# Performance work log

Measured on AMD Instinct MI355X. Metric: run time of the kernel, lower is better.

The kernel has to match this reference:

```python
import jax, jax.numpy as jnp
import numpy as np

N_ENT = 100000
N_REL = 16
DIM = 128
N_LAYERS = 2
N_BASES = 4
N_EDGES = 640000
BATCH = 1024
N_NEG = 64
BN_EPS = 1e-5


def setup_inputs() -> dict:
    key = jax.random.key(0)
    ks = jax.random.split(key, 16)
    inp = {
        'head_idx': jax.random.randint(ks[0], (BATCH,), 0, N_ENT),
        'relation_idx': jax.random.randint(ks[1], (BATCH,), 0, N_REL),
        'tail_idx': jax.random.randint(ks[2], (BATCH,), 0, N_ENT),
        'negative_idx': jax.random.randint(ks[3], (BATCH, N_NEG), 0, N_ENT),
        'edge_index': jax.random.randint(ks[4], (2, N_EDGES), 0, N_ENT),
        'edge_type': jax.random.randint(ks[5], (N_EDGES,), 0, N_REL),
        # learned parameters (xavier-ish scaling)
        'entity_table': jax.random.normal(ks[6], (N_ENT, DIM), jnp.float32) * 0.02,
        'relation_table': jax.random.normal(ks[7], (N_REL, DIM), jnp.float32) * 0.02,
        'bases': jax.random.normal(ks[8], (N_LAYERS, N_BASES, DIM, DIM), jnp.float32) * (1.0 / np.sqrt(DIM)),
        'coeffs': jax.random.normal(ks[9], (N_LAYERS, N_REL, N_BASES), jnp.float32) * 0.5,
        'w_sl': jax.random.normal(ks[10], (N_LAYERS, DIM, DIM), jnp.float32) * (1.0 / np.sqrt(DIM)),
        'b_sl': jnp.zeros((N_LAYERS, DIM), jnp.float32),
        'gamma': jnp.ones((N_LAYERS, DIM), jnp.float32),
        'beta': jnp.zeros((N_LAYERS, DIM), jnp.float32),
    }
    return inp


def _encode(entity_table, bases, coeffs, w_sl, b_sl, gamma, beta, edge_index, edge_type):
    src, dst = edge_index[0], edge_index[1]
    n = entity_table.shape[0]
    # degree normalization (same dst for every layer)
    deg = jnp.zeros((n,), entity_table.dtype).at[dst].add(1.0)
    deg = jnp.maximum(deg, 1.0)[:, None]
    x = entity_table
    for l in range(N_LAYERS):
        # basis decomposition: W[r] = sum_b coeff[r,b] * bases[b]
        W = jnp.einsum('rb,bij->rij', coeffs[l], bases[l])  # [R, d, d]
        out = x @ w_sl[l] + b_sl[l]  # self-loop linear
        # transform all nodes under every relation once, then gather per edge
        H = jnp.einsum('nd,rdf->rnf', x, W)  # [R, N, d]
        msg = H[edge_type, src]  # [E, d]
        out = out.at[dst].add(msg)
        out = out / deg
        # BatchNorm1d (training mode: biased batch stats over nodes)
        mu = jnp.mean(out, axis=0)
        var = jnp.var(out, axis=0)
        out = (out - mu) * jax.lax.rsqrt(var + BN_EPS) * gamma[l] + beta[l]
        x = jax.nn.relu(out)
    return x


def reference(head_idx, relation_idx, tail_idx, negative_idx, edge_index, edge_type,
              entity_table, relation_table, bases, coeffs, w_sl, b_sl, gamma, beta):
    ent = _encode(entity_table, bases, coeffs, w_sl, b_sl, gamma, beta, edge_index, edge_type)
    head = ent[head_idx]                      # [B, d]
    rel = relation_table[relation_idx]        # [B, d]
    tail = ent[tail_idx]                      # [B, d]
    neg = ent[negative_idx]                   # [B, K, d]
    d_pos = head + rel - tail
    pos_score = -jnp.sqrt(jnp.sum(d_pos * d_pos, axis=-1))
    d_neg = (head + rel)[:, None, :] - neg
    neg_score = -jnp.sqrt(jnp.sum(d_neg * d_neg, axis=-1))
    return pos_score, neg_score
```

## Files before the change

kernel.cpp:

```cpp
#include <hip/hip_runtime.h>
#include <stdint.h>

#define N_ENTS  100000
#define N_RELS  16
#define DIM     128
#define NB      4
#define TILE_U  10240
#define NEDGE   640000
#define BATCH   1024
#define NNEG    64
#define BN_EPS  1e-5f
#define BCAP    64
#define NPB     32
#define NBLK2   3125
#define CONVX_BLKS 6250
#define CONVP_BLKS 652

#define P_REL    0
#define P_BASES  2048
#define P_COEFF  133120
#define P_WSL    133248
#define P_BSL    166016
#define P_GAMMA  166272
#define P_BETA   166528
#define P_TOTAL  166784

typedef unsigned int uint;
typedef short short8 __attribute__((ext_vector_type(8)));
typedef float f4 __attribute__((ext_vector_type(4)));

__device__ __forceinline__ float bf2f(unsigned short u) {
    return __uint_as_float(((unsigned int)u) << 16);
}
__device__ __forceinline__ float bflo(unsigned int u) { return __uint_as_float(u << 16); }
__device__ __forceinline__ float bfhi(unsigned int u) { return __uint_as_float(u & 0xffff0000u); }
__device__ __forceinline__ unsigned short f2bf(float f) {
    unsigned int x = __float_as_uint(f);
    x += 0x7fffu + ((x >> 16) & 1u);
    return (unsigned short)(x >> 16);
}
__device__ __forceinline__ unsigned int pack2(float a, float b) {
    return (unsigned int)f2bf(a) | ((unsigned int)f2bf(b) << 16);
}

__device__ __forceinline__ int bf16_like(unsigned int h) {
    unsigned int m = h & 0x7FFFu;
    return (m == 0u) || (m >= 0x2D00u && m < 0x4400u);
}
__global__ __launch_bounds__(256) void k_detect(const unsigned int* __restrict__ ent,
                                                int* __restrict__ flag) {
    __shared__ int cnt[256];
    unsigned int u = ent[threadIdx.x];
    cnt[threadIdx.x] = bf16_like(u & 0xFFFFu) & bf16_like(u >> 16);
    __syncthreads();
    for (int s = 128; s > 0; s >>= 1) {
        if (threadIdx.x < s) cnt[threadIdx.x] += cnt[threadIdx.x + s];
        __syncthreads();
    }
    if (threadIdx.x == 0) flag[0] = (cnt[0] >= 140) ? 1 : 0;
}

__device__ __forceinline__ unsigned short cvt1(const void* src, int i, int isbf) {
    return isbf ? ((const unsigned short*)src)[i] : f2bf(((const float*)src)[i]);
}
__global__ __launch_bounds__(256) void k_conv(
    const void* __restrict__ src, unsigned short* __restrict__ xrow,
    const void* __restrict__ rtab, const void* __restrict__ bases,
    const void* __restrict__ coeffs, const void* __restrict__ wsl,
    const void* __restrict__ bsl, const void* __restrict__ gamma,
    const void* __restrict__ beta,
    unsigned short* __restrict__ par, const int* __restrict__ flag)
{
    const int isbf = flag[0];
    if (blockIdx.x < CONVX_BLKS) {
        if (isbf) return;
        const int kc = threadIdx.x >> 4, r = threadIdx.x & 15;
        const int n = blockIdx.x * 16 + r;
        const size_t e0 = (size_t)n * DIM + kc * 8;
        const float4 f0 = *(const float4*)((const float*)src + e0);
        const float4 f1 = *(const float4*)((const float*)src + e0 + 4);
        uint4 w;
        w.x = pack2(f0.x, f0.y); w.y = pack2(f0.z, f0.w);
        w.z = pack2(f1.x, f1.y); w.w = pack2(f1.z, f1.w);
        *(uint4*)(xrow + e0) = w;
        return;
    }
    const int i = (blockIdx.x - CONVX_BLKS) * 256 + threadIdx.x;
    if (i >= P_TOTAL) return;
    unsigned short v;
    if      (i < P_BASES)  v = cvt1(rtab,   i - P_REL,    isbf);
    else if (i < P_COEFF)  v = cvt1(bases,  i - P_BASES,  isbf);
    else if (i < P_WSL)    v = cvt1(coeffs, i - P_COEFF,  isbf);
    else if (i < P_BSL)    v = cvt1(wsl,    i - P_WSL,    isbf);
    else if (i < P_GAMMA)  v = cvt1(bsl,    i - P_BSL,    isbf);
    else if (i < P_BETA)   v = cvt1(gamma,  i - P_GAMMA,  isbf);
    else                   v = cvt1(beta,   i - P_BETA,   isbf);
    par[i] = v;
}

__global__ __launch_bounds__(256) void k_fillB(const int* __restrict__ src, const int* __restrict__ dst,
                                               const int* __restrict__ et, int* __restrict__ cnt,
                                               uint* __restrict__ bucket) {
    const int e = blockIdx.x * 256 + threadIdx.x;
    const int d = dst[e];
    const int p = atomicAdd(&cnt[d], 1);
    if (p < BCAP) bucket[(size_t)d * BCAP + p] = (uint)src[e] | ((uint)et[e] << 20);
}

__global__ __launch_bounds__(256) void k_transw2(const unsigned short* __restrict__ par,
                                                 unsigned short* __restrict__ WtT,
                                                 float* __restrict__ cf32) {
    if (blockIdx.x == 80) {
        const int i = threadIdx.x;
        if (i < 2 * 17 * 4) {
            const int l = i / 68, rem = i - l * 68, r = rem >> 2, b = rem & 3;
            cf32[i] = (r < N_RELS) ? bf2f(par[P_COEFF + l * N_RELS * NB + r * NB + b]) : 0.f;
        }
        return;
    }
    const int i = blockIdx.x * 256 + threadIdx.x;
    const int l = i / 10240;
    const int rem = i - l * 10240;
    const int jt2 = rem / 1280;
    const int rem2 = rem - jt2 * 1280;
    const int kc = rem2 >> 4, r = rem2 & 15;
    const int n = jt2 * 16 + r;
    unsigned short v[8];
#pragma unroll
    for (int e = 0; e < 8; ++e) {
        const int k = kc * 8 + e;
        v[e] = (k < DIM)
            ? par[P_WSL + l * DIM * DIM + k * DIM + n]
            : par[P_BASES + l * NB * DIM * DIM + (k - DIM) * DIM + n];
    }
    *(uint4*)(WtT + (size_t)l * 81920 + (size_t)jt2 * TILE_U + (size_t)kc * 128 + r * 8) = *(uint4*)v;
}

__global__ __launch_bounds__(256, 4) void k_fused(
    const uint* __restrict__ bucket, const int* __restrict__ cnt,
    const float* __restrict__ cf, const unsigned short* __restrict__ xin,
    const void* __restrict__ ent, const int* __restrict__ flag, const int lay,
    const float* __restrict__ stp, const unsigned short* __restrict__ gprev,
    const unsigned short* __restrict__ bprev,
    const unsigned short* __restrict__ wtT, const unsigned short* __restrict__ bsl,
    unsigned short* __restrict__ out, float* __restrict__ pstats)
{
    __shared__ unsigned short Ash[NPB * 640];
    const int tid = threadIdx.x;
    const int wave = tid >> 6, lane = tid & 63;
    const int n0 = blockIdx.x * NPB;
    const float inv_n = 1.0f / (float)N_ENTS;

    const unsigned short* __restrict__ xs =
        (lay == 0 && flag[0]) ? (const unsigned short*)ent : xin;

    float gnA = 1.f, ofA = 0.f, gnB = 1.f, ofB = 0.f, flr = -3.0e38f;
    if (lay) {
        const int f0 = lane * 2, f1 = f0 + 1;
        const float mu0 = stp[f0] * inv_n, mu1 = stp[f1] * inv_n;
        const float va0 = stp[DIM + f0] * inv_n - mu0 * mu0;
        const float va1 = stp[DIM + f1] * inv_n - mu1 * mu1;
        gnA = bf2f(gprev[f0]) * rsqrtf(va0 + BN_EPS); ofA = bf2f(bprev[f0]) - mu0 * gnA;
        gnB = bf2f(gprev[f1]) * rsqrtf(va1 + BN_EPS); ofB = bf2f(bprev[f1]) - mu1 * gnB;
        flr = 0.f;
    }

    {
        const int r = tid >> 3, c = tid & 7;
        const size_t e0 = (size_t)(n0 + r) * DIM + c * 8;
        uint4 v0 = *(const uint4*)(xs + e0);
        uint4 v1 = *(const uint4*)(xs + e0 + 64);
        if (lay) {
            uint vv[8] = {v0.x, v0.y, v0.z, v0.w, v1.x, v1.y, v1.z, v1.w};
#pragma unroll
            for (int p = 0; p < 8; ++p) {
                const int f0 = c * 8 + (p >> 2) * 64 + (p & 3) * 2;
                const float mu0 = stp[f0] * inv_n, mu1 = stp[f0 + 1] * inv_n;
                const float va0 = stp[DIM + f0] * inv_n - mu0 * mu0;
                const float va1 = stp[DIM + f0 + 1] * inv_n - mu1 * mu1;
                const float g0 = bf2f(gprev[f0]) * rsqrtf(va0 + BN_EPS);
                const float g1 = bf2f(gprev[f0 + 1]) * rsqrtf(va1 + BN_EPS);
                const float o0 = bf2f(bprev[f0]) - mu0 * g0;
                const float o1 = bf2f(bprev[f0 + 1]) - mu1 * g1;
                const float w0 = fmaxf(fmaf(bflo(vv[p]), g0, o0), 0.f);
                const float w1 = fmaxf(fmaf(bfhi(vv[p]), g1, o1), 0.f);
                vv[p] = pack2(w0, w1);
            }
            v0.x = vv[0]; v0.y = vv[1]; v0.z = vv[2]; v0.w = vv[3];
            v1.x = vv[4]; v1.y = vv[5]; v1.z = vv[6]; v1.w = vv[7];
        }
        const int byte0 = (r * 1280 + c * 16) ^ ((r & 7) << 4);
        *(uint4*)((char*)Ash + byte0) = v0;
        *(uint4*)((char*)Ash + byte0 + 128) = v1;
    }

    const uint* __restrict__ x32 = (const uint*)xs;
    const int mybase = n0 + wave * 8;
    for (int pr = 0; pr < 4; ++pr) {
        const int na = mybase + pr * 2;
        int ca = cnt[na];     if (ca > BCAP) ca = BCAP;
        int cb = cnt[na + 1]; if (cb > BCAP) cb = BCAP;
        const int qm = ((ca > cb ? ca : cb) + 7) >> 3;
        float aLo[2][NB] = {{0.f,0.f,0.f,0.f},{0.f,0.f,0.f,0.f}};
        float aHi[2][NB] = {{0.f,0.f,0.f,0.f},{0.f,0.f,0.f,0.f}};
        const uint4* __restrict__ bk = (const uint4*)(bucket + (size_t)na * BCAP);
        for (int j = 0; j < qm; ++j) {
            uint rec[2][8];
            uint xw[2][8];
            const int b8 = j * 8;
#pragma unroll
            for (int h = 0; h < 2; ++h) {
                const int cn = h ? cb : ca;
                if (b8 < cn) {
                    const uint4 r0 = bk[h * 16 + j * 2];
                    const uint4 r1 = bk[h * 16 + j * 2 + 1];
                    rec[h][0] = r0.x; rec[h][1] = r0.y; rec[h][2] = r0.z; rec[h][3] = r0.w;
                    rec[h][4] = r1.x; rec[h][5] = r1.y; rec[h][6] = r1.z; rec[h][7] = r1.w;
#pragma unroll
                    for (int s = 0; s < 8; ++s) {
                        uint rr = (uint)__builtin_amdgcn_readfirstlane((int)rec[h][s]);
                        if (b8 + s >= cn) rr = 0x01000000u;
                        rec[h][s] = rr;
                        xw[h][s] = x32[(size_t)(rr & 0xFFFFFu) * 64 + lane];
                    }
                }
            }
#pragma unroll
            for (int h = 0; h < 2; ++h) {
                const int cn = h ? cb : ca;
                if (b8 < cn) {
#pragma unroll
                    for (int s = 0; s < 8; ++s) {
                        const int rel = (int)(rec[h][s] >> 20);
                        const float4 cc = *(const float4*)(cf + rel * 4);
                        const float xl = fmaxf(fmaf(bflo(xw[h][s]), gnA, ofA), flr);
                        const float xh = fmaxf(fmaf(bfhi(xw[h][s]), gnB, ofB), flr);
                        aLo[h][0] = fmaf(cc.x, xl, aLo[h][0]);
                        aHi[h][0] = fmaf(cc.x, xh, aHi[h][0]);
                        aLo[h][1] = fmaf(cc.y, xl, aLo[h][1]);
                        aHi[h][1] = fmaf(cc.y, xh, aHi[h][1]);
                        aLo[h][2] = fmaf(cc.z, xl, aLo[h][2]);
                        aHi[h][2] = fmaf(cc.z, xh, aHi[h][2]);
                        aLo[h][3] = fmaf(cc.w, xl, aLo[h][3]);
                        aHi[h][3] = fmaf(cc.w, xh, aHi[h][3]);
                    }
                }
            }
        }
#pragma unroll
        for (int h = 0; h < 2; ++h) {
            const int ra = wave * 8 + pr * 2 + h;
            const int swz = (ra & 7) << 4;
#pragma unroll
            for (int b = 0; b < NB; ++b) {
                const int byte = (ra * 1280 + 256 + b * 256 + lane * 4) ^ swz;
                *(uint*)((char*)Ash + byte) = pack2(aLo[h][b], aHi[h][b]);
            }
        }
    }

    const int quad = lane >> 4, l16 = lane & 15;
    f4 acc[2][2];
#pragma unroll
    for (int i = 0; i < 2; ++i)
#pragma unroll
        for (int j = 0; j < 2; ++j)
#pragma unroll
            for (int r = 0; r < 4; ++r) acc[i][j][r] = 0.f;

    const unsigned short* __restrict__ pB0 = wtT + (size_t)(2 * wave) * TILE_U + quad * 128 + l16 * 8;
    const unsigned short* __restrict__ pB1 = pB0 + TILE_U;
    const char* Ab = (const char*)Ash;
    const int swz = (l16 & 7) << 4;
    const int b0e = (l16 * 1280 + quad * 16) ^ swz;
    const int b0o = (l16 * 1280 + 64 + quad * 16) ^ swz;
    const int b1e = ((l16 + 16) * 1280 + quad * 16) ^ swz;
    const int b1o = ((l16 + 16) * 1280 + 64 + quad * 16) ^ swz;

    short8 xa0, xa1, xb0, xb1, ya0, ya1, yb0, yb1;
#define FLDA(P, s) \
    P##a0 = *(const short8*)(Ab + (((s) & 1) ? b0o : b0e) + ((s) >> 1) * 128); \
    P##a1 = *(const short8*)(Ab + (((s) & 1) ? b1o : b1e) + ((s) >> 1) * 128);
#define FLDB(P, s) \
    P##b0 = *(const short8*)(pB0 + (s) * 512); \
    P##b1 = *(const short8*)(pB1 + (s) * 512);
#define FLD(P, s) FLDA(P, s) FLDB(P, s)
#define FMM(P) \
    acc[0][0] = __builtin_amdgcn_mfma_f32_16x16x32_bf16(P##a0, P##b0, acc[0][0], 0, 0, 0); \
    acc[0][1] = __builtin_amdgcn_mfma_f32_16x16x32_bf16(P##a0, P##b1, acc[0][1], 0, 0, 0); \
    acc[1][0] = __builtin_amdgcn_mfma_f32_16x16x32_bf16(P##a1, P##b0, acc[1][0], 0, 0, 0); \
    acc[1][1] = __builtin_amdgcn_mfma_f32_16x16x32_bf16(P##a1, P##b1, acc[1][1], 0, 0, 0);

    FLDB(x, 0) FLDB(y, 1)
    __syncthreads();
    FLDA(x, 0) FLDA(y, 1)
    FMM(x) FLD(x, 2)
    FMM(y) FLD(y, 3)
    FMM(x) FLD(x, 4)
    FMM(y) FLD(y, 5)
    FMM(x) FLD(x, 6)
    FMM(y) FLD(y, 7)
    FMM(x) FLD(x, 8)
    FMM(y) FLD(y, 9)
    FMM(x) FLD(x, 10)
    FMM(y) FLD(y, 11)
    FMM(x) FLD(x, 12)
    FMM(y) FLD(y, 13)
    FMM(x) FLD(x, 14)
    FMM(y) FLD(y, 15)
    FMM(x) FLD(x, 16)
    FMM(y) FLD(y, 17)
    FMM(x) FLD(x, 18)
    FMM(y) FLD(y, 19)
    FMM(x)
    FMM(y)
#undef FLDA
#undef FLDB
#undef FLD
#undef FMM

    float ssum[2] = {0.f, 0.f}, sssq[2] = {0.f, 0.f};
#pragma unroll
    for (int m = 0; m < 2; ++m) {
#pragma unroll
        for (int r = 0; r < 4; ++r) {
            const int row = n0 + m * 16 + quad * 4 + r;
            const float rdeg = 1.0f / fmaxf((float)cnt[row], 1.0f);
#pragma unroll
            for (int n = 0; n < 2; ++n) {
                const int col = (2 * wave + n) * 16 + l16;
                const float o = (acc[m][n][r] + bf2f(bsl[col])) * rdeg;
                out[(size_t)row * DIM + col] = f2bf(o);
                ssum[n] += o;
                sssq[n] += o * o;
            }
        }
    }
#pragma unroll
    for (int n = 0; n < 2; ++n) {
        float s = ssum[n], q2 = sssq[n];
        s += __shfl_xor(s, 16, 64);  s += __shfl_xor(s, 32, 64);
        q2 += __shfl_xor(q2, 16, 64); q2 += __shfl_xor(q2, 32, 64);
        if (quad == 0) {
            const int col = (2 * wave + n) * 16 + l16;
            pstats[(size_t)blockIdx.x * 256 + col] = s;
            pstats[(size_t)blockIdx.x * 256 + 128 + col] = q2;
        }
    }
}

__global__ __launch_bounds__(256) void k_stats(const float* __restrict__ pstats,
                                               float* __restrict__ st) {
    const int o = threadIdx.x;
    const int b0 = blockIdx.x * 25;
    float s = 0.f;
    for (int b = b0; b < b0 + 25; ++b)
        s += pstats[(size_t)b * 256 + o];
    atomicAdd(&st[o], s);
}

__global__ __launch_bounds__(256) void k_score(
    const int* __restrict__ head, const int* __restrict__ rel,
    const int* __restrict__ tail, const int* __restrict__ negi,
    const unsigned short* __restrict__ emb, const unsigned short* __restrict__ rtab,
    const float* __restrict__ st1, const unsigned short* __restrict__ gm1,
    const unsigned short* __restrict__ bt1,
    void* __restrict__ outp, const int* __restrict__ flag)
{
    const int wave = threadIdx.x >> 6, lane = threadIdx.x & 63;
    const int w = blockIdx.x * 4 + wave;
    const float inv_n = 1.0f / (float)N_ENTS;
    const int f0 = lane * 2, f1 = f0 + 1;
    const float mu0 = st1[f0] * inv_n, mu1 = st1[f1] * inv_n;
    const float va0 = st1[DIM + f0] * inv_n - mu0 * mu0;
    const float va1 = st1[DIM + f1] * inv_n - mu1 * mu1;
    const float g0 = bf2f(gm1[f0]) * rsqrtf(va0 + BN_EPS);
    const float g1 = bf2f(gm1[f1]) * rsqrtf(va1 + BN_EPS);
    const float o0 = bf2f(bt1[f0]) - mu0 * g0;
    const float o1 = bf2f(bt1[f1]) - mu1 * g1;

    int i, t;
    if (w < BATCH) { i = w; t = tail[w]; }
    else { const int w2 = w - BATCH; i = w2 >> 6; t = negi[w2]; }
    const uint hv = ((const uint*)emb)[(size_t)head[i] * 64 + lane];
    const uint rv = ((const uint*)rtab)[(size_t)rel[i] * 64 + lane];
    const uint tv = ((const uint*)emb)[(size_t)t * 64 + lane];
    const float h0 = fmaxf(fmaf(bflo(hv), g0, o0), 0.f);
    const float h1 = fmaxf(fmaf(bfhi(hv), g1, o1), 0.f);
    const float t0 = fmaxf(fmaf(bflo(tv), g0, o0), 0.f);
    const float t1 = fmaxf(fmaf(bfhi(tv), g1, o1), 0.f);
    const float d0 = (h0 + bflo(rv)) - t0;
    const float d1 = (h1 + bfhi(rv)) - t1;
    float s = d0 * d0 + d1 * d1;
#pragma unroll
    for (int m = 32; m >= 1; m >>= 1) s += __shfl_xor(s, m, 64);
    if (lane == 0) {
        const float v = -sqrtf(s);
        if (flag[0]) ((unsigned short*)outp)[w] = f2bf(v);
        else         ((float*)outp)[w] = v;
    }
}

extern "C" void kernel_launch(void* const* d_in, const int* in_sizes, int n_in,
                              void* d_out, int out_size, void* d_ws, size_t ws_size,
                              hipStream_t stream)
{
    const int* head = (const int*)d_in[0];
    const int* rel  = (const int*)d_in[1];
    const int* tail = (const int*)d_in[2];
    const int* negi = (const int*)d_in[3];
    const int* eidx = (const int*)d_in[4];
    const int* etyp = (const int*)d_in[5];
    const void* ent_tab = d_in[6];
    const void* rtab_in = d_in[7];
    const void* bases_in = d_in[8];
    const void* coeffs_in = d_in[9];
    const void* wsl_in = d_in[10];
    const void* bsl_in = d_in[11];
    const void* gamma_in = d_in[12];
    const void* beta_in = d_in[13];

    char* ws = (char*)d_ws;
    size_t off = 0;
    auto alloc = [&](size_t bytes) -> char* {
        char* p = ws + off;
        off += (bytes + 511) & ~(size_t)511;
        return p;
    };
    int* flag            = (int*)alloc(4);
    int* cnt             = (int*)alloc((size_t)N_ENTS * 4);
    uint* bucket         = (uint*)alloc((size_t)N_ENTS * BCAP * 4);
    unsigned short* xrow = (unsigned short*)alloc((size_t)N_ENTS * DIM * 2);
    unsigned short* outA = (unsigned short*)alloc((size_t)N_ENTS * DIM * 2);
    unsigned short* outB = (unsigned short*)alloc((size_t)N_ENTS * DIM * 2);
    unsigned short* par  = (unsigned short*)alloc((size_t)P_TOTAL * 2);
    unsigned short* WtT  = (unsigned short*)alloc((size_t)2 * 81920 * 2);
    float* cf32          = (float*)alloc((size_t)2 * 17 * 4 * 4);
    float* pstats        = (float*)alloc((size_t)NBLK2 * 256 * 4);
    float* stats         = (float*)alloc(2 * 2 * DIM * 4);
    (void)ws_size; (void)in_sizes; (void)n_in; (void)out_size;

    const int* esrc = eidx;
    const int* edst = eidx + NEDGE;

    k_detect<<<1, 256, 0, stream>>>((const unsigned int*)ent_tab, flag);

    k_conv<<<CONVX_BLKS + CONVP_BLKS, 256, 0, stream>>>(
        ent_tab, xrow, rtab_in, bases_in, coeffs_in, wsl_in, bsl_in, gamma_in, beta_in,
        par, flag);
    k_transw2<<<81, 256, 0, stream>>>(par, WtT, cf32);

    hipMemsetAsync(cnt, 0, (size_t)N_ENTS * 4, stream);
    hipMemsetAsync(stats, 0, 2 * 2 * DIM * 4, stream);

    k_fillB<<<NEDGE / 256, 256, 0, stream>>>(esrc, edst, etyp, cnt, bucket);

    for (int l = 0; l < 2; ++l) {
        const unsigned short* bl = par + P_BSL + l * DIM;
        const unsigned short* wt = WtT + (size_t)l * 81920;
        const float* cf = cf32 + l * 68;

        k_fused<<<NBLK2, 256, 0, stream>>>(
            bucket, cnt, cf,
            l ? outA : xrow, ent_tab, flag, l,
            stats , par + P_GAMMA, par + P_BETA,
            wt, bl, l ? outB : outA, pstats);
        k_stats<<<125, 256, 0, stream>>>(pstats, stats + l * 2 * DIM);
    }

    k_score<<<(BATCH + BATCH * NNEG) / 4, 256, 0, stream>>>(
        head, rel, tail, negi, outB, par + P_REL,
        stats + 2 * DIM, par + P_GAMMA + DIM, par + P_BETA + DIM,
        d_out, flag);
}
```

Baseline: 354.0 us.

## Template fused layer kernel on layer and gather four nodes per iteration

Makes the layer index a template parameter, so the first layer skips the BN/ReLU transform in the gather loop and the floor trick goes away. Each wave now gathers neighbour rows for four nodes per iteration instead of two, which puts more independent global loads in flight to hide gather latency. The launch bounds also drop the min-blocks hint. The cost is higher register pressure from the 4x8 staging arrays and accumulators, which may reduce occupancy. Imbalanced degrees across the four nodes can also waste iterations.

After: 408.4 us. +15.4%, slower.

```diff
diff --git a/kernel.cpp b/kernel.cpp
--- a/kernel.cpp
+++ b/kernel.cpp
@@ -11,6 +11,7 @@
 #define NNEG    64
 #define BN_EPS  1e-5f
 #define BCAP    64
+#define SENTR   0x01000000u
 #define NPB     32
 #define NBLK2   3125
 #define CONVX_BLKS 6250
@@ -136,10 +137,11 @@
     *(uint4*)(WtT + (size_t)l * 81920 + (size_t)jt2 * TILE_U + (size_t)kc * 128 + r * 8) = *(uint4*)v;
 }
 
-__global__ __launch_bounds__(256, 4) void k_fused(
+template<int LAY>
+__global__ __launch_bounds__(256) void k_fused(
     const uint* __restrict__ bucket, const int* __restrict__ cnt,
     const float* __restrict__ cf, const unsigned short* __restrict__ xin,
-    const void* __restrict__ ent, const int* __restrict__ flag, const int lay,
+    const void* __restrict__ ent, const int* __restrict__ flag,
     const float* __restrict__ stp, const unsigned short* __restrict__ gprev,
     const unsigned short* __restrict__ bprev,
     const unsigned short* __restrict__ wtT, const unsigned short* __restrict__ bsl,
@@ -152,17 +154,16 @@
     const float inv_n = 1.0f / (float)N_ENTS;
 
     const unsigned short* __restrict__ xs =
-        (lay == 0 && flag[0]) ? (const unsigned short*)ent : xin;
-
-    float gnA = 1.f, ofA = 0.f, gnB = 1.f, ofB = 0.f, flr = -3.0e38f;
-    if (lay) {
+        (LAY == 0 && flag[0]) ? (const unsigned short*)ent : xin;
+
+    float gnA = 1.f, ofA = 0.f, gnB = 1.f, ofB = 0.f;
+    if (LAY) {
         const int f0 = lane * 2, f1 = f0 + 1;
         const float mu0 = stp[f0] * inv_n, mu1 = stp[f1] * inv_n;
         const float va0 = stp[DIM + f0] * inv_n - mu0 * mu0;
         const float va1 = stp[DIM + f1] * inv_n - mu1 * mu1;
         gnA = bf2f(gprev[f0]) * rsqrtf(va0 + BN_EPS); ofA = bf2f(bprev[f0]) - mu0 * gnA;
         gnB = bf2f(gprev[f1]) * rsqrtf(va1 + BN_EPS); ofB = bf2f(bprev[f1]) - mu1 * gnB;
-        flr = 0.f;
     }
 
     {
@@ -170,7 +171,7 @@
         const size_t e0 = (size_t)(n0 + r) * DIM + c * 8;
         uint4 v0 = *(const uint4*)(xs + e0);
         uint4 v1 = *(const uint4*)(xs + e0 + 64);
-        if (lay) {
+        if (LAY) {
             uint vv[8] = {v0.x, v0.y, v0.z, v0.w, v1.x, v1.y, v1.z, v1.w};
 #pragma unroll
             for (int p = 0; p < 8; ++p) {
@@ -196,65 +197,82 @@
 
     const uint* __restrict__ x32 = (const uint*)xs;
     const int mybase = n0 + wave * 8;
-    for (int pr = 0; pr < 4; ++pr) {
-        const int na = mybase + pr * 2;
-        int ca = cnt[na];     if (ca > BCAP) ca = BCAP;
-        int cb = cnt[na + 1]; if (cb > BCAP) cb = BCAP;
-        const int qm = ((ca > cb ? ca : cb) + 7) >> 3;
-        float aLo[2][NB] = {{0.f,0.f,0.f,0.f},{0.f,0.f,0.f,0.f}};
-        float aHi[2][NB] = {{0.f,0.f,0.f,0.f},{0.f,0.f,0.f,0.f}};
-        const uint4* __restrict__ bk = (const uint4*)(bucket + (size_t)na * BCAP);
+    for (int pp = 0; pp < 2; ++pp) {
+        const int naA = mybase + pp * 4;
+        const int naB = naA + 2;
+        int cA0 = cnt[naA];     if (cA0 > BCAP) cA0 = BCAP;
+        int cA1 = cnt[naA + 1]; if (cA1 > BCAP) cA1 = BCAP;
+        int cB0 = cnt[naB];     if (cB0 > BCAP) cB0 = BCAP;
+        int cB1 = cnt[naB + 1]; if (cB1 > BCAP) cB1 = BCAP;
+        const int qm0 = ((cA0 > cA1 ? cA0 : cA1) + 7) >> 3;
+        const int qm1 = ((cB0 > cB1 ? cB0 : cB1) + 7) >> 3;
+        const int qm = qm0 > qm1 ? qm0 : qm1;
+        float accLo[4][NB] = {{0.f,0.f,0.f,0.f},{0.f,0.f,0.f,0.f},
+                              {0.f,0.f,0.f,0.f},{0.f,0.f,0.f,0.f}};
+        float accHi[4][NB] = {{0.f,0.f,0.f,0.f},{0.f,0.f,0.f,0.f},
+                              {0.f,0.f,0.f,0.f},{0.f,0.f,0.f,0.f}};
+        const uint4* __restrict__ bkA = (const uint4*)(bucket + (size_t)naA * BCAP);
+        const uint4* __restrict__ bkB = (const uint4*)(bucket + (size_t)naB * BCAP);
         for (int j = 0; j < qm; ++j) {
-            uint rec[2][8];
-            uint xw[2][8];
             const int b8 = j * 8;
-#pragma unroll
-            for (int h = 0; h < 2; ++h) {
-                const int cn = h ? cb : ca;
+            uint rec[4][8];
+            uint xw[4][8];
+            const int cns[4] = {cA0, cA1, cB0, cB1};
+#pragma unroll
+            for (int g = 0; g < 4; ++g) {
+                const int cn = cns[g];
                 if (b8 < cn) {
+                    const uint4* bk = (g < 2) ? bkA : bkB;
+                    const int h = g & 1;
                     const uint4 r0 = bk[h * 16 + j * 2];
                     const uint4 r1 = bk[h * 16 + j * 2 + 1];
-                    rec[h][0] = r0.x; rec[h][1] = r0.y; rec[h][2] = r0.z; rec[h][3] = r0.w;
-                    rec[h][4] = r1.x; rec[h][5] = r1.y; rec[h][6] = r1.z; rec[h][7] = r1.w;
+                    rec[g][0] = r0.x; rec[g][1] = r0.y; rec[g][2] = r0.z; rec[g][3] = r0.w;
+                    rec[g][4] = r1.x; rec[g][5] = r1.y; rec[g][6] = r1.z; rec[g][7] = r1.w;
 #pragma unroll
                     for (int s = 0; s < 8; ++s) {
-                        uint rr = (uint)__builtin_amdgcn_readfirstlane((int)rec[h][s]);
-                        if (b8 + s >= cn) rr = 0x01000000u;
-                        rec[h][s] = rr;
-                        xw[h][s] = x32[(size_t)(rr & 0xFFFFFu) * 64 + lane];
+                        uint rr = (uint)__builtin_amdgcn_readfirstlane((int)rec[g][s]);
+                        if (b8 + s >= cn) rr = SENTR;
+                        rec[g][s] = rr;
+                        xw[g][s] = x32[(size_t)(rr & 0xFFFFFu) * 64 + lane];
                     }
                 }
             }
 #pragma unroll
-            for (int h = 0; h < 2; ++h) {
-                const int cn = h ? cb : ca;
+            for (int g = 0; g < 4; ++g) {
+                const int cn = cns[g];
                 if (b8 < cn) {
 #pragma unroll
                     for (int s = 0; s < 8; ++s) {
-                        const int rel = (int)(rec[h][s] >> 20);
+                        const int rel = (int)(rec[g][s] >> 20);
                         const float4 cc = *(const float4*)(cf + rel * 4);
-                        const float xl = fmaxf(fmaf(bflo(xw[h][s]), gnA, ofA), flr);
-                        const float xh = fmaxf(fmaf(bfhi(xw[h][s]), gnB, ofB), flr);
-                        aLo[h][0] = fmaf(cc.x, xl, aLo[h][0]);
-                        aHi[h][0] = fmaf(cc.x, xh, aHi[h][0]);
-                        aLo[h][1] = fmaf(cc.y, xl, aLo[h][1]);
-                        aHi[h][1] = fmaf(cc.y, xh, aHi[h][1]);
-                        aLo[h][2] = fmaf(cc.z, xl, aLo[h][2]);
-                        aHi[h][2] = fmaf(cc.z, xh, aHi[h][2]);
-                        aLo[h][3] = fmaf(cc.w, xl, aLo[h][3]);
-                        aHi[h][3] = fmaf(cc.w, xh, aHi[h][3]);
+                        float xl, xh;
+                        if (LAY) {
+                            xl = fmaxf(fmaf(bflo(xw[g][s]), gnA, ofA), 0.f);
+                            xh = fmaxf(fmaf(bfhi(xw[g][s]), gnB, ofB), 0.f);
+                        } else {
+                            xl = bflo(xw[g][s]);
+                            xh = bfhi(xw[g][s]);
+                        }
+                        accLo[g][0] = fmaf(cc.x, xl, accLo[g][0]);
+                        accHi[g][0] = fmaf(cc.x, xh, accHi[g][0]);
+                        accLo[g][1] = fmaf(cc.y, xl, accLo[g][1]);
+                        accHi[g][1] = fmaf(cc.y, xh, accHi[g][1]);
+                        accLo[g][2] = fmaf(cc.z, xl, accLo[g][2]);
+                        accHi[g][2] = fmaf(cc.z, xh, accHi[g][2]);
+                        accLo[g][3] = fmaf(cc.w, xl, accLo[g][3]);
+                        accHi[g][3] = fmaf(cc.w, xh, accHi[g][3]);
                     }
                 }
             }
         }
 #pragma unroll
-        for (int h = 0; h < 2; ++h) {
-            const int ra = wave * 8 + pr * 2 + h;
+        for (int g = 0; g < 4; ++g) {
+            const int ra = wave * 8 + pp * 4 + g;
             const int swz = (ra & 7) << 4;
 #pragma unroll
             for (int b = 0; b < NB; ++b) {
                 const int byte = (ra * 1280 + 256 + b * 256 + lane * 4) ^ swz;
-                *(uint*)((char*)Ash + byte) = pack2(aLo[h][b], aHi[h][b]);
+                *(uint*)((char*)Ash + byte) = pack2(accLo[g][b], accHi[g][b]);
             }
         }
     }
@@ -455,18 +473,17 @@
 
     k_fillB<<<NEDGE / 256, 256, 0, stream>>>(esrc, edst, etyp, cnt, bucket);
 
-    for (int l = 0; l < 2; ++l) {
-        const unsigned short* bl = par + P_BSL + l * DIM;
-        const unsigned short* wt = WtT + (size_t)l * 81920;
-        const float* cf = cf32 + l * 68;
-
-        k_fused<<<NBLK2, 256, 0, stream>>>(
-            bucket, cnt, cf,
-            l ? outA : xrow, ent_tab, flag, l,
-            stats , par + P_GAMMA, par + P_BETA,
-            wt, bl, l ? outB : outA, pstats);
-        k_stats<<<125, 256, 0, stream>>>(pstats, stats + l * 2 * DIM);
-    }
+    k_fused<0><<<NBLK2, 256, 0, stream>>>(
+        bucket, cnt, cf32, xrow, ent_tab, flag,
+        stats, par + P_GAMMA, par + P_BETA,
+        WtT, par + P_BSL, outA, pstats);
+    k_stats<<<125, 256, 0, stream>>>(pstats, stats);
+
+    k_fused<1><<<NBLK2, 256, 0, stream>>>(
+        bucket, cnt, cf32 + 68, outA, ent_tab, flag,
+        stats, par + P_GAMMA, par + P_BETA,
+        WtT + 81920, par + P_BSL + DIM, outB, pstats);
+    k_stats<<<125, 256, 0, stream>>>(pstats, stats + 2 * DIM);
 
     k_score<<<(BATCH + BATCH * NNEG) / 4, 256, 0, stream>>>(
         head, rel, tail, negi, outB, par + P_REL,
```
